# Optimization experiments

Hardware: AMD Instinct MI355X
Metric: run time of the kernel (lower is better)

The kernel has to match this reference:

```python
import jax, jax.numpy as jnp
import numpy as np

# dims: B=4 batch, S=512 seq, P=128 input_size, C=64 classes(=hidden_size), K=64 gln layer width, 4 context bits -> 16 contexts
B, S, P, C, K, NBITS = 4, 512, 128, 64, 64, 4
NCTX = 2 ** NBITS
LOGIT_CLIP = 5.0


def setup_inputs() -> dict:
    key = jax.random.key(0)
    ks = jax.random.split(key, 8)
    return {
        "x": jax.random.normal(ks[0], (B, S, P), jnp.float32),
        "hidden": jax.random.normal(ks[1], (B, C), jnp.float32),
        # GLN layer 1: per-class, per-neuron halfspace context hyperplanes and gated weights
        "H1": jax.random.normal(ks[2], (C, K, NBITS, P), jnp.float32),
        "W1": jax.random.normal(ks[3], (C, K, NCTX, P), jnp.float32) / np.sqrt(P),
        # GLN output layer: one neuron per class
        "H2": jax.random.normal(ks[4], (C, NBITS, P), jnp.float32),
        "W2": jax.random.normal(ks[5], (C, NCTX, K), jnp.float32) / np.sqrt(K),
        # fc2: Linear(input_size, hidden_size)
        "fc2_w": jax.random.normal(ks[6], (C, P), jnp.float32) / np.sqrt(P),
        "fc2_b": jnp.zeros((C,), jnp.float32),
    }


def _ctx_index(bits):
    # bits: (..., NBITS) bool -> integer context id in [0, 2^NBITS)
    return (bits * (2 ** jnp.arange(NBITS, dtype=jnp.int32))).sum(-1)


def _gln_predict(x, H1, W1, H2, W2):
    # base predictions: sigmoid(x) -> logit space is x itself (clipped for stability)
    l0 = jnp.clip(x, -LOGIT_CLIP, LOGIT_CLIP)  # (B,S,P)
    # layer 1: halfspace gating then geometric mixing in logit space
    ctx1 = _ctx_index(jnp.einsum('bsp,ckjp->bsckj', x, H1) > 0)          # (B,S,C,K)
    mix1 = jnp.einsum('bsp,ckxp->bsckx', l0, W1)                          # (B,S,C,K,NCTX)
    l1 = jnp.take_along_axis(mix1, ctx1[..., None], axis=-1)[..., 0]      # (B,S,C,K)
    l1 = jnp.clip(l1, -LOGIT_CLIP, LOGIT_CLIP)
    # output layer: one gated neuron per class
    ctx2 = _ctx_index(jnp.einsum('bsp,cjp->bscj', x, H2) > 0)             # (B,S,C)
    mix2 = jnp.einsum('bsck,cxk->bscx', l1, W2)                           # (B,S,C,NCTX)
    l2 = jnp.take_along_axis(mix2, ctx2[..., None], axis=-1)[..., 0]      # (B,S,C)
    return jax.nn.sigmoid(l2)


def reference(x, hidden, H1, W1, H2, W2, fc2_w, fc2_b):
    b = _gln_predict(x, H1, W1, H2, W2)                   # (B,S,C)
    # multihead gating
    sig_alphas = jax.nn.sigmoid(x @ fc2_w.T + fc2_b)      # (B,S,C)
    b = b * sig_alphas

    # sequential roll+add+relu recurrence over seq_len
    def step(h, bt):
        h = jax.nn.relu(bt + jnp.roll(h, 1, axis=-1))
        return h, h

    h_last, outs = jax.lax.scan(step, hidden, jnp.swapaxes(b, 0, 1))  # outs: (S,B,C)
    outputs = jnp.swapaxes(outs, 0, 1)                                # (B,S,C)
    return outputs, h_last
```

## Files before the change

### kernel.cpp

```cpp
#include <hip/hip_runtime.h>
#include <math.h>

#define BB 4
#define SS 512
#define PP 128
#define CC 64
#define KK 64
#define NCTX_ 16
#define TT 64
#define NTILES ((BB*SS)/TT)

typedef __attribute__((ext_vector_type(8))) short bf16x8;
typedef __attribute__((ext_vector_type(4))) float f32x4;

static __device__ __forceinline__ float bf2f(short h) {
    unsigned u = ((unsigned)(unsigned short)h) << 16;
    return __builtin_bit_cast(float, u);
}
static __device__ __forceinline__ short f2bf(float f) {
    unsigned u = __builtin_bit_cast(unsigned, f);
    unsigned r = (u + 0x7fffu + ((u >> 16) & 1u)) >> 16;
    return (short)(unsigned short)r;
}
static __device__ __forceinline__ bf16x8 clampfrag(bf16x8 h) {
    typedef __attribute__((ext_vector_type(4))) unsigned u32x4;
    u32x4 u = __builtin_bit_cast(u32x4, h);
    #pragma unroll
    for (int i = 0; i < 4; ++i) {
        const unsigned w = u[i];
        const unsigned s = w & 0x80008000u;
        unsigned lo = w & 0x7fffu;
        unsigned hi = (w >> 16) & 0x7fffu;
        lo = lo > 0x40a0u ? 0x40a0u : lo;
        hi = hi > 0x40a0u ? 0x40a0u : hi;
        u[i] = s | lo | (hi << 16);
    }
    return __builtin_bit_cast(bf16x8, u);
}

__global__ __launch_bounds__(256) void h1pack_kernel(const float* __restrict__ H1,
                                                     short* __restrict__ H1h,
                                                     short* __restrict__ H1l)
{
    const int lane = threadIdx.x & 63;
    const int gw   = blockIdx.x * 4 + (threadIdx.x >> 6);
    const int row  = (gw >> 2) * 16 + (lane >> 2);
    const int col  = (gw & 3) * 32 + (lane & 3) * 8;
    const float4* src = reinterpret_cast<const float4*>(H1 + (size_t)row * PP + col);
    const float4 v0 = src[0], v1 = src[1];
    const float vv[8] = {v0.x, v0.y, v0.z, v0.w, v1.x, v1.y, v1.z, v1.w};
    bf16x8 hh, ll;
    #pragma unroll
    for (int e = 0; e < 8; ++e) {
        const short hv = f2bf(vv[e]);
        hh[e] = hv;
        ll[e] = f2bf(vv[e] - bf2f(hv));
    }
    const int lp = (lane & 3) * 16 + (lane >> 2);
    const size_t o = ((size_t)gw * 64 + lp) * 8;
    *reinterpret_cast<bf16x8*>(H1h + o) = hh;
    *reinterpret_cast<bf16x8*>(H1l + o) = ll;
}

__global__ __launch_bounds__(256) void w1pack_kernel(const float* __restrict__ W1,
                                                     short* __restrict__ W1h)
{
    const int lane = threadIdx.x & 63;
    const int q    = threadIdx.x >> 6;
    const int tile = blockIdx.x;
    const float4* src = reinterpret_cast<const float4*>(
        W1 + ((size_t)tile * 16 + (lane >> 2)) * PP + q * 32 + (lane & 3) * 8);
    const float4 v0 = src[0], v1 = src[1];
    const float vv[8] = {v0.x, v0.y, v0.z, v0.w, v1.x, v1.y, v1.z, v1.w};
    bf16x8 hh;
    #pragma unroll
    for (int e = 0; e < 8; ++e) hh[e] = f2bf(vv[e]);
    const int lp = (lane & 3) * 16 + (lane >> 2);
    const size_t o = (((size_t)tile * 4 + q) * 64 + lp) * 8;
    *reinterpret_cast<bf16x8*>(W1h + o) = hh;
}

__global__ __launch_bounds__(256) void h2wpack_kernel(const float* __restrict__ H2,
                                                      const float* __restrict__ fc2w,
                                                      short* __restrict__ Hh,
                                                      short* __restrict__ Hl)
{
    const int cidx = blockIdx.x;
    const int q    = threadIdx.x >> 6;
    const int l    = threadIdx.x & 63;
    const int row  = l & 15;
    const int col  = q * 32 + (l >> 4) * 8;
    float vv[8];
    if (row < 4) {
        const float4* s = reinterpret_cast<const float4*>(
            H2 + ((size_t)cidx * 4 + row) * PP + col);
        const float4 a = s[0], b = s[1];
        vv[0]=a.x; vv[1]=a.y; vv[2]=a.z; vv[3]=a.w;
        vv[4]=b.x; vv[5]=b.y; vv[6]=b.z; vv[7]=b.w;
    } else if (row == 4) {
        const float4* s = reinterpret_cast<const float4*>(
            fc2w + (size_t)cidx * PP + col);
        const float4 a = s[0], b = s[1];
        vv[0]=a.x; vv[1]=a.y; vv[2]=a.z; vv[3]=a.w;
        vv[4]=b.x; vv[5]=b.y; vv[6]=b.z; vv[7]=b.w;
    } else {
        #pragma unroll
        for (int e = 0; e < 8; ++e) vv[e] = 0.f;
    }
    bf16x8 hh, ll;
    #pragma unroll
    for (int e = 0; e < 8; ++e) {
        const short hv = f2bf(vv[e]);
        hh[e] = hv;
        ll[e] = f2bf(vv[e] - bf2f(hv));
    }
    const size_t o = (((size_t)cidx * 4 + q) * 64 + l) * 8;
    *reinterpret_cast<bf16x8*>(Hh + o) = hh;
    *reinterpret_cast<bf16x8*>(Hl + o) = ll;
}

__global__ __launch_bounds__(256, 4) void predict_kernel(
    const float* __restrict__ x,
    const short* __restrict__ H1h,
    const short* __restrict__ H1l,
    const short* __restrict__ W1h,
    const short* __restrict__ H2Wh,
    const short* __restrict__ H2Wl,
    const float* __restrict__ W2,
    const float* __restrict__ fc2b,
    float* __restrict__ bout)
{
    __shared__ short xuh[4][4][64][8];
    __shared__ short xul[4][4][64][8];
    __shared__ unsigned char ctxb[TT][68];
    __shared__ unsigned char bit2b[TT];
    __shared__ float af[TT];

    const int tid  = threadIdx.x;
    const int lane = tid & 63;
    const int wid  = __builtin_amdgcn_readfirstlane(tid >> 6);
    const int bid  = blockIdx.x;
    const int sw   = ((bid & 7) << 8) | (bid >> 3);
    const int c    = sw >> 5;
    const int tile = sw & (NTILES - 1);
    const int tok0 = tile * TT;

    const int t15 = lane & 15;
    const int g   = lane >> 4;
    const f32x4 zero4 = {0.f, 0.f, 0.f, 0.f};

    {
        const int tok = tid >> 2;
        const int q   = tid & 3;
        const int tl  = tok & 15;
        const int jj  = tok >> 4;
        const float4* x4 = reinterpret_cast<const float4*>(
            x + (size_t)(tok0 + tok) * PP + q * 32);
        float v[32];
        #pragma unroll
        for (int i = 0; i < 8; ++i) {
            const float4 t = x4[i];
            v[i*4+0]=t.x; v[i*4+1]=t.y; v[i*4+2]=t.z; v[i*4+3]=t.w;
        }
        #pragma unroll
        for (int gg = 0; gg < 4; ++gg) {
            bf16x8 hh, ll;
            #pragma unroll
            for (int e = 0; e < 8; ++e) {
                const float f = v[gg*8+e];
                const short hv = f2bf(f);
                hh[e] = hv;
                ll[e] = f2bf(f - bf2f(hv));
            }
            *reinterpret_cast<bf16x8*>(&xuh[jj][q][gg*16 + tl][0]) = hh;
            *reinterpret_cast<bf16x8*>(&xul[jj][q][gg*16 + tl][0]) = ll;
        }
    }
    __syncthreads();

    const int ctile = c * 16 + wid * 4;
    #pragma unroll
    for (int half = 0; half < 2; ++half) {
        f32x4 acc[4][2];
        #pragma unroll
        for (int nt = 0; nt < 4; ++nt) { acc[nt][0] = zero4; acc[nt][1] = zero4; }
        #pragma unroll
        for (int q = 0; q < 4; ++q) {
            bf16x8 bh[2], bl[2];
            #pragma unroll
            for (int j2 = 0; j2 < 2; ++j2) {
                const int j = half * 2 + j2;
                bh[j2] = *reinterpret_cast<const bf16x8*>(&xuh[j][q][lane][0]);
                bl[j2] = *reinterpret_cast<const bf16x8*>(&xul[j][q][lane][0]);
            }
            #pragma unroll
            for (int nt = 0; nt < 4; ++nt) {
                const size_t fo = (((size_t)(ctile + nt) * 4 + q) * 64 + lane) * 8;
                const bf16x8 ah = *reinterpret_cast<const bf16x8*>(H1h + fo);
                const bf16x8 al = *reinterpret_cast<const bf16x8*>(H1l + fo);
                #pragma unroll
                for (int j2 = 0; j2 < 2; ++j2) {
                    acc[nt][j2] = __builtin_amdgcn_mfma_f32_16x16x32_bf16(ah, bh[j2], acc[nt][j2], 0, 0, 0);
                    acc[nt][j2] = __builtin_amdgcn_mfma_f32_16x16x32_bf16(ah, bl[j2], acc[nt][j2], 0, 0, 0);
                    acc[nt][j2] = __builtin_amdgcn_mfma_f32_16x16x32_bf16(al, bh[j2], acc[nt][j2], 0, 0, 0);
                }
            }
        }
        #pragma unroll
        for (int nt = 0; nt < 4; ++nt) {
            #pragma unroll
            for (int j2 = 0; j2 < 2; ++j2) {
                const int tok = half * 32 + j2 * 16 + t15;
                const int k   = wid * 16 + nt * 4 + g;
                const int cv  = (acc[nt][j2][0] > 0.f ? 1 : 0) |
                                (acc[nt][j2][1] > 0.f ? 2 : 0) |
                                (acc[nt][j2][2] > 0.f ? 4 : 0) |
                                (acc[nt][j2][3] > 0.f ? 8 : 0);
                ctxb[tok][k] = (unsigned char)cv;
            }
        }
    }

    {
        f32x4 a2 = zero4;
        #pragma unroll
        for (int q = 0; q < 4; ++q) {
            const bf16x8 bh = *reinterpret_cast<const bf16x8*>(&xuh[wid][q][lane][0]);
            const bf16x8 bl = *reinterpret_cast<const bf16x8*>(&xul[wid][q][lane][0]);
            const size_t fo = (((size_t)(c * 4 + q)) * 64 + lane) * 8;
            const bf16x8 ah = *reinterpret_cast<const bf16x8*>(H2Wh + fo);
            const bf16x8 al = *reinterpret_cast<const bf16x8*>(H2Wl + fo);
            a2 = __builtin_amdgcn_mfma_f32_16x16x32_bf16(ah, bh, a2, 0, 0, 0);
            a2 = __builtin_amdgcn_mfma_f32_16x16x32_bf16(ah, bl, a2, 0, 0, 0);
            a2 = __builtin_amdgcn_mfma_f32_16x16x32_bf16(al, bh, a2, 0, 0, 0);
        }
        const int tok = wid * 16 + t15;
        if (g == 0) {
            bit2b[tok] = (unsigned char)((a2[0] > 0.f ? 1 : 0) | (a2[1] > 0.f ? 2 : 0) |
                                         (a2[2] > 0.f ? 4 : 0) | (a2[3] > 0.f ? 8 : 0));
        } else if (g == 1) {
            af[tok] = a2[0];
        }
    }
    __syncthreads();

    short* l1s = &xul[0][0][0][0];
    {
        bf16x8 ch[4][4];
        #pragma unroll
        for (int j = 0; j < 4; ++j)
            #pragma unroll
            for (int q = 0; q < 4; ++q)
                ch[j][q] = clampfrag(*reinterpret_cast<const bf16x8*>(&xuh[j][q][lane][0]));

        #pragma unroll 4
        for (int k16 = 0; k16 < 16; ++k16) {
            const int k = wid * 16 + k16;
            f32x4 acc[4] = {zero4, zero4, zero4, zero4};
            #pragma unroll
            for (int q = 0; q < 4; ++q) {
                const size_t fo = (((size_t)(c * KK + k) * 4 + q) * 64 + lane) * 8;
                const bf16x8 ah = *reinterpret_cast<const bf16x8*>(W1h + fo);
                #pragma unroll
                for (int j = 0; j < 4; ++j)
                    acc[j] = __builtin_amdgcn_mfma_f32_16x16x32_bf16(ah, ch[j][q], acc[j], 0, 0, 0);
            }
            #pragma unroll
            for (int j = 0; j < 4; ++j) {
                const int tok = j * 16 + t15;
                const int cx  = ctxb[tok][k];
                const int sel = cx & 3;
                const float v = (sel == 0) ? acc[j][0] : (sel == 1) ? acc[j][1] :
                                (sel == 2) ? acc[j][2] : acc[j][3];
                if (g == (cx >> 2))
                    l1s[tok * 68 + k] = f2bf(fminf(fmaxf(v, -5.f), 5.f));
            }
        }
    }
    __syncthreads();

    {
        const int tok = tid >> 2;
        const int qt  = tid & 3;
        const int ctx2 = bit2b[tok];
        const float4* w2p = reinterpret_cast<const float4*>(
            W2 + ((size_t)c * NCTX_ + ctx2) * KK + qt * 16);
        float s = 0.f;
        #pragma unroll
        for (int i4 = 0; i4 < 4; ++i4) {
            const float4 w = w2p[i4];
            const int kb = tok * 68 + qt * 16 + i4 * 4;
            s = fmaf(w.x, bf2f(l1s[kb + 0]),
                fmaf(w.y, bf2f(l1s[kb + 1]),
                fmaf(w.z, bf2f(l1s[kb + 2]),
                fmaf(w.w, bf2f(l1s[kb + 3]), s))));
        }
        s += __shfl_xor(s, 1, 64);
        s += __shfl_xor(s, 2, 64);
        if (qt == 0) {
            const float alpha = af[tok] + fc2b[c];
            const float bv = (1.f / (1.f + expf(-s))) * (1.f / (1.f + expf(-alpha)));
            bout[(size_t)(tok0 + tok) * CC + c] = bv;
        }
    }
}

__global__ __launch_bounds__(256, 4) void predict_fb_kernel(
    const float* __restrict__ x,
    const float* __restrict__ H1,
    const float* __restrict__ W1b,
    const float* __restrict__ H2,
    const float* __restrict__ W2,
    const float* __restrict__ fc2w,
    const float* __restrict__ fc2b,
    float* __restrict__ bout)
{
    __shared__ float xs[PP][TT + 1];
    __shared__ float bitss[4][TT];
    __shared__ float apart[4][TT];
    __shared__ float l2part[4][TT];

    const int tid  = threadIdx.x;
    const int lane = tid & 63;
    const int wid  = __builtin_amdgcn_readfirstlane(tid >> 6);
    const int bid  = blockIdx.x;
    const int sw   = ((bid & 7) << 8) | (bid >> 3);
    const int c    = sw >> 5;
    const int tile = sw & (NTILES - 1);
    const int tok0 = tile * TT;

    {
        const float4* xg = reinterpret_cast<const float4*>(x + (size_t)tok0 * PP);
        #pragma unroll
        for (int it = 0; it < (TT * PP / 4) / 256; ++it) {
            const int i = it * 256 + tid;
            const float4 v = xg[i];
            const int t = i >> 5;
            const int p = (i & 31) << 2;
            xs[p + 0][t] = v.x; xs[p + 1][t] = v.y;
            xs[p + 2][t] = v.z; xs[p + 3][t] = v.w;
        }
    }
    __syncthreads();

    int ctxreg[16];
    {
        const float4* H1c4 = reinterpret_cast<const float4*>(H1 + (size_t)c * KK * 4 * PP);
        #pragma unroll
        for (int gg = 0; gg < 8; ++gg) {
            const int k = wid * 16 + gg * 2;
            const float4* h4 = H1c4 + (size_t)k * 4 * 32;
            float acc[8] = {0.f, 0.f, 0.f, 0.f, 0.f, 0.f, 0.f, 0.f};
            #pragma unroll 2
            for (int p4 = 0; p4 < 32; ++p4) {
                const float x0 = xs[4 * p4 + 0][lane];
                const float x1 = xs[4 * p4 + 1][lane];
                const float x2 = xs[4 * p4 + 2][lane];
                const float x3 = xs[4 * p4 + 3][lane];
                #pragma unroll
                for (int r = 0; r < 8; ++r) {
                    const float4 w = h4[r * 32 + p4];
                    acc[r] = fmaf(w.w, x3, fmaf(w.z, x2, fmaf(w.y, x1, fmaf(w.x, x0, acc[r]))));
                }
            }
            ctxreg[gg * 2]     = (acc[0] > 0.f ? 1 : 0) | (acc[1] > 0.f ? 2 : 0) |
                                 (acc[2] > 0.f ? 4 : 0) | (acc[3] > 0.f ? 8 : 0);
            ctxreg[gg * 2 + 1] = (acc[4] > 0.f ? 1 : 0) | (acc[5] > 0.f ? 2 : 0) |
                                 (acc[6] > 0.f ? 4 : 0) | (acc[7] > 0.f ? 8 : 0);
        }
    }
    {
        const float4* h2 = reinterpret_cast<const float4*>(H2 + ((size_t)c * 4 + wid) * PP);
        float d = 0.f;
        #pragma unroll 8
        for (int p4 = 0; p4 < 32; ++p4) {
            const float4 w = h2[p4];
            d = fmaf(w.w, xs[4 * p4 + 3][lane], fmaf(w.z, xs[4 * p4 + 2][lane],
                fmaf(w.y, xs[4 * p4 + 1][lane], fmaf(w.x, xs[4 * p4 + 0][lane], d))));
        }
        bitss[wid][lane] = (d > 0.f) ? 1.f : 0.f;
        const float4* fw = reinterpret_cast<const float4*>(fc2w + (size_t)c * PP) + wid * 8;
        float ap = 0.f;
        #pragma unroll
        for (int p4 = 0; p4 < 8; ++p4) {
            const float4 w = fw[p4];
            const int p = wid * 32 + 4 * p4;
            ap = fmaf(w.w, xs[p + 3][lane], fmaf(w.z, xs[p + 2][lane],
                 fmaf(w.y, xs[p + 1][lane], fmaf(w.x, xs[p + 0][lane], ap))));
        }
        apart[wid][lane] = ap;
    }
    __syncthreads();

    float l1v[16];
    {
        const float4* W1c4 = reinterpret_cast<const float4*>(W1b) +
                             (size_t)(c * KK + wid * 16) * 512;
        #pragma unroll
        for (int gg = 0; gg < 2; ++gg) {
            float s[8] = {0.f, 0.f, 0.f, 0.f, 0.f, 0.f, 0.f, 0.f};
            const float4* wp[8];
            #pragma unroll
            for (int jj = 0; jj < 8; ++jj) {
                const int kk = gg * 8 + jj;
                wp[jj] = W1c4 + (size_t)kk * 512 + (size_t)ctxreg[kk] * 32;
            }
            #pragma unroll 2
            for (int p4 = 0; p4 < 32; ++p4) {
                const float x0 = fminf(fmaxf(xs[4 * p4 + 0][lane], -5.f), 5.f);
                const float x1 = fminf(fmaxf(xs[4 * p4 + 1][lane], -5.f), 5.f);
                const float x2 = fminf(fmaxf(xs[4 * p4 + 2][lane], -5.f), 5.f);
                const float x3 = fminf(fmaxf(xs[4 * p4 + 3][lane], -5.f), 5.f);
                #pragma unroll
                for (int jj = 0; jj < 8; ++jj) {
                    const float4 wv = wp[jj][p4];
                    s[jj] = fmaf(wv.w, x3, fmaf(wv.z, x2, fmaf(wv.y, x1, fmaf(wv.x, x0, s[jj]))));
                }
            }
            #pragma unroll
            for (int jj = 0; jj < 8; ++jj)
                l1v[gg * 8 + jj] = fminf(fmaxf(s[jj], -5.f), 5.f);
        }
    }
    {
        const int ctx2 = (bitss[0][lane] > 0.5f ? 1 : 0) | (bitss[1][lane] > 0.5f ? 2 : 0) |
                         (bitss[2][lane] > 0.5f ? 4 : 0) | (bitss[3][lane] > 0.5f ? 8 : 0);
        const float* w2 = W2 + ((size_t)c * NCTX_ + ctx2) * KK + wid * 16;
        float lp = 0.f;
        #pragma unroll
        for (int jj = 0; jj < 16; ++jj) lp = fmaf(w2[jj], l1v[jj], lp);
        l2part[wid][lane] = lp;
    }
    __syncthreads();
    if (wid == 0) {
        const int t = lane;
        const float l2 = (l2part[0][t] + l2part[1][t]) + (l2part[2][t] + l2part[3][t]);
        const float alpha = apart[0][t] + apart[1][t] + apart[2][t] + apart[3][t] + fc2b[c];
        const float bv = (1.f / (1.f + expf(-l2))) * (1.f / (1.f + expf(-alpha)));
        bout[(size_t)(tok0 + t) * CC + c] = bv;
    }
}

__global__ __launch_bounds__(64) void scan_kernel(const float* __restrict__ hidden,
                                                  float* __restrict__ out)
{
    const int b    = blockIdx.x;
    const int lane = threadIdx.x;
    float* row = out + (size_t)b * SS * CC;
    const float hprev = hidden[b * CC + ((lane + 63) & 63)];

    float nb[64];
    #pragma unroll
    for (int j = 0; j < 64; ++j) nb[j] = row[j * CC + ((lane + j) & 63)];
    float acc = fmaxf(nb[0] + hprev, 0.f);
    row[lane] = acc;
    #pragma unroll
    for (int j = 1; j < 64; ++j) {
        acc += nb[j];
        row[j * CC + ((lane + j) & 63)] = acc;
    }
    for (int c0 = 64; c0 < SS; c0 += 64) {
        #pragma unroll
        for (int j = 0; j < 64; ++j)
            nb[j] = row[(c0 + j) * CC + ((lane + c0 + j) & 63)];
        #pragma unroll
        for (int j = 0; j < 64; ++j) {
            acc += nb[j];
            row[(c0 + j) * CC + ((lane + c0 + j) & 63)] = acc;
        }
    }
    out[(size_t)BB * SS * CC + b * CC + ((lane + 63) & 63)] = acc;
}

extern "C" void kernel_launch(void* const* d_in, const int* in_sizes, int n_in,
                              void* d_out, int out_size, void* d_ws, size_t ws_size,
                              hipStream_t stream) {
    const float* x      = (const float*)d_in[0];
    const float* hidden = (const float*)d_in[1];
    const float* H1     = (const float*)d_in[2];
    const float* W1     = (const float*)d_in[3];
    const float* H2     = (const float*)d_in[4];
    const float* W2     = (const float*)d_in[5];
    const float* fc2w   = (const float*)d_in[6];
    const float* fc2b   = (const float*)d_in[7];
    float* out = (float*)d_out;

    const size_t MB = 1024 * 1024;

    if (ws_size >= 25 * MB) {
        short* W1hp = (short*)d_ws;
        short* H1hp = (short*)((char*)d_ws + 16 * MB);
        short* H1lp = (short*)((char*)d_ws + 20 * MB);
        short* H2Whp = (short*)((char*)d_ws + 24 * MB);
        short* H2Wlp = (short*)((char*)d_ws + 24 * MB + 256 * 1024);
        w1pack_kernel<<<dim3(CC * KK), 256, 0, stream>>>(W1, W1hp);
        h1pack_kernel<<<dim3(1024), 256, 0, stream>>>(H1, H1hp, H1lp);
        h2wpack_kernel<<<dim3(CC), 256, 0, stream>>>(H2, fc2w, H2Whp, H2Wlp);
        predict_kernel<<<dim3(CC * NTILES), 256, 0, stream>>>(
            x, H1hp, H1lp, W1hp, H2Whp, H2Wlp, W2, fc2b, out);
    } else {
        predict_fb_kernel<<<dim3(CC * NTILES), 256, 0, stream>>>(
            x, H1, W1, H2, W2, fc2w, fc2b, out);
    }
    scan_kernel<<<dim3(BB), 64, 0, stream>>>(hidden, out);
}
```

Before: 110.2 us.

## Use 32x32x16 MFMA for gating projections and merge pack kernels into one launch

The H1 and H2/fc2 gating projections move from 16x16x32 to 32x32x16 bf16 MFMA tiles. The shared-memory x fragments and the packed H1/H2 weight layouts are reorganised to match, and the W1 path re-indexes into the new layout. The three weight-packing kernels become a single launch, cutting launch overhead and making fewer, larger MFMA calls. In exchange the accumulators are larger (16 floats each), which raises register pressure under the occupancy-4 launch bound, and the H2 projection now runs on only two of the four waves.

```diff
diff --git a/kernel.cpp b/kernel.cpp
--- a/kernel.cpp
+++ b/kernel.cpp
@@ -12,6 +12,7 @@
 
 typedef __attribute__((ext_vector_type(8))) short bf16x8;
 typedef __attribute__((ext_vector_type(4))) float f32x4;
+typedef __attribute__((ext_vector_type(16))) float f32x16;
 
 static __device__ __forceinline__ float bf2f(short h) {
     unsigned u = ((unsigned)(unsigned short)h) << 16;
@@ -38,91 +39,87 @@
     return __builtin_bit_cast(bf16x8, u);
 }
 
-__global__ __launch_bounds__(256) void h1pack_kernel(const float* __restrict__ H1,
-                                                     short* __restrict__ H1h,
-                                                     short* __restrict__ H1l)
+__global__ __launch_bounds__(256) void pack_kernel(
+    const float* __restrict__ W1, const float* __restrict__ H1,
+    const float* __restrict__ H2, const float* __restrict__ fc2w,
+    short* __restrict__ W1h, short* __restrict__ H1h32, short* __restrict__ H1l32,
+    short* __restrict__ H2Wh, short* __restrict__ H2Wl)
 {
+    const int bid  = blockIdx.x;
+    const int w    = threadIdx.x >> 6;
     const int lane = threadIdx.x & 63;
-    const int gw   = blockIdx.x * 4 + (threadIdx.x >> 6);
-    const int row  = (gw >> 2) * 16 + (lane >> 2);
-    const int col  = (gw & 3) * 32 + (lane & 3) * 8;
-    const float4* src = reinterpret_cast<const float4*>(H1 + (size_t)row * PP + col);
-    const float4 v0 = src[0], v1 = src[1];
-    const float vv[8] = {v0.x, v0.y, v0.z, v0.w, v1.x, v1.y, v1.z, v1.w};
-    bf16x8 hh, ll;
-    #pragma unroll
-    for (int e = 0; e < 8; ++e) {
-        const short hv = f2bf(vv[e]);
-        hh[e] = hv;
-        ll[e] = f2bf(vv[e] - bf2f(hv));
-    }
-    const int lp = (lane & 3) * 16 + (lane >> 2);
-    const size_t o = ((size_t)gw * 64 + lp) * 8;
-    *reinterpret_cast<bf16x8*>(H1h + o) = hh;
-    *reinterpret_cast<bf16x8*>(H1l + o) = ll;
-}
-
-__global__ __launch_bounds__(256) void w1pack_kernel(const float* __restrict__ W1,
-                                                     short* __restrict__ W1h)
-{
-    const int lane = threadIdx.x & 63;
-    const int q    = threadIdx.x >> 6;
-    const int tile = blockIdx.x;
-    const float4* src = reinterpret_cast<const float4*>(
-        W1 + ((size_t)tile * 16 + (lane >> 2)) * PP + q * 32 + (lane & 3) * 8);
-    const float4 v0 = src[0], v1 = src[1];
-    const float vv[8] = {v0.x, v0.y, v0.z, v0.w, v1.x, v1.y, v1.z, v1.w};
-    bf16x8 hh;
-    #pragma unroll
-    for (int e = 0; e < 8; ++e) hh[e] = f2bf(vv[e]);
-    const int lp = (lane & 3) * 16 + (lane >> 2);
-    const size_t o = (((size_t)tile * 4 + q) * 64 + lp) * 8;
-    *reinterpret_cast<bf16x8*>(W1h + o) = hh;
-}
-
-__global__ __launch_bounds__(256) void h2wpack_kernel(const float* __restrict__ H2,
-                                                      const float* __restrict__ fc2w,
-                                                      short* __restrict__ Hh,
-                                                      short* __restrict__ Hl)
-{
-    const int cidx = blockIdx.x;
-    const int q    = threadIdx.x >> 6;
-    const int l    = threadIdx.x & 63;
-    const int row  = l & 15;
-    const int col  = q * 32 + (l >> 4) * 8;
-    float vv[8];
-    if (row < 4) {
-        const float4* s = reinterpret_cast<const float4*>(
-            H2 + ((size_t)cidx * 4 + row) * PP + col);
+
+    if (bid < CC * KK) {
+        const int tile = bid;
+        const int q    = w;
+        const float4* src = reinterpret_cast<const float4*>(
+            W1 + ((size_t)tile * 16 + (lane >> 2)) * PP + q * 32 + (lane & 3) * 8);
+        const float4 v0 = src[0], v1 = src[1];
+        const float vv[8] = {v0.x, v0.y, v0.z, v0.w, v1.x, v1.y, v1.z, v1.w};
+        bf16x8 hh;
+        #pragma unroll
+        for (int e = 0; e < 8; ++e) hh[e] = f2bf(vv[e]);
+        const int lp = (lane & 3) * 16 + (lane >> 2);
+        *reinterpret_cast<bf16x8*>(W1h + (((size_t)tile * 4 + q) * 64 + lp) * 8) = hh;
+    } else if (bid < CC * KK + 1024) {
+        const int gw  = (bid - CC * KK) * 4 + w;
+        const int row = (gw >> 3) * 32 + (lane & 31);
+        const int col = (gw & 7) * 16 + (lane >> 5) * 8;
+        const float4* s = reinterpret_cast<const float4*>(H1 + (size_t)row * PP + col);
         const float4 a = s[0], b = s[1];
-        vv[0]=a.x; vv[1]=a.y; vv[2]=a.z; vv[3]=a.w;
-        vv[4]=b.x; vv[5]=b.y; vv[6]=b.z; vv[7]=b.w;
-    } else if (row == 4) {
-        const float4* s = reinterpret_cast<const float4*>(
-            fc2w + (size_t)cidx * PP + col);
-        const float4 a = s[0], b = s[1];
-        vv[0]=a.x; vv[1]=a.y; vv[2]=a.z; vv[3]=a.w;
-        vv[4]=b.x; vv[5]=b.y; vv[6]=b.z; vv[7]=b.w;
+        const float vv[8] = {a.x, a.y, a.z, a.w, b.x, b.y, b.z, b.w};
+        bf16x8 hh, ll;
+        #pragma unroll
+        for (int e = 0; e < 8; ++e) {
+            const short hv = f2bf(vv[e]);
+            hh[e] = hv;
+            ll[e] = f2bf(vv[e] - bf2f(hv));
+        }
+        const size_t o = ((size_t)gw * 64 + lane) * 8;
+        *reinterpret_cast<bf16x8*>(H1h32 + o) = hh;
+        *reinterpret_cast<bf16x8*>(H1l32 + o) = ll;
     } else {
-        #pragma unroll
-        for (int e = 0; e < 8; ++e) vv[e] = 0.f;
-    }
-    bf16x8 hh, ll;
-    #pragma unroll
-    for (int e = 0; e < 8; ++e) {
-        const short hv = f2bf(vv[e]);
-        hh[e] = hv;
-        ll[e] = f2bf(vv[e] - bf2f(hv));
-    }
-    const size_t o = (((size_t)cidx * 4 + q) * 64 + l) * 8;
-    *reinterpret_cast<bf16x8*>(Hh + o) = hh;
-    *reinterpret_cast<bf16x8*>(Hl + o) = ll;
+        const int cidx = bid - (CC * KK + 1024);
+        #pragma unroll
+        for (int i = 0; i < 2; ++i) {
+            const int q8  = w * 2 + i;
+            const int row = lane & 31;
+            const int col = q8 * 16 + (lane >> 5) * 8;
+            float vv[8];
+            if (row < 4) {
+                const float4* s = reinterpret_cast<const float4*>(
+                    H2 + ((size_t)cidx * 4 + row) * PP + col);
+                const float4 a = s[0], b = s[1];
+                vv[0]=a.x; vv[1]=a.y; vv[2]=a.z; vv[3]=a.w;
+                vv[4]=b.x; vv[5]=b.y; vv[6]=b.z; vv[7]=b.w;
+            } else if (row == 4) {
+                const float4* s = reinterpret_cast<const float4*>(
+                    fc2w + (size_t)cidx * PP + col);
+                const float4 a = s[0], b = s[1];
+                vv[0]=a.x; vv[1]=a.y; vv[2]=a.z; vv[3]=a.w;
+                vv[4]=b.x; vv[5]=b.y; vv[6]=b.z; vv[7]=b.w;
+            } else {
+                #pragma unroll
+                for (int e = 0; e < 8; ++e) vv[e] = 0.f;
+            }
+            bf16x8 hh, ll;
+            #pragma unroll
+            for (int e = 0; e < 8; ++e) {
+                const short hv = f2bf(vv[e]);
+                hh[e] = hv;
+                ll[e] = f2bf(vv[e] - bf2f(hv));
+            }
+            const size_t o = (((size_t)cidx * 8 + q8) * 64 + lane) * 8;
+            *reinterpret_cast<bf16x8*>(H2Wh + o) = hh;
+            *reinterpret_cast<bf16x8*>(H2Wl + o) = ll;
+        }
+    }
 }
 
 __global__ __launch_bounds__(256, 4) void predict_kernel(
     const float* __restrict__ x,
-    const short* __restrict__ H1h,
-    const short* __restrict__ H1l,
+    const short* __restrict__ H1h32,
+    const short* __restrict__ H1l32,
     const short* __restrict__ W1h,
     const short* __restrict__ H2Wh,
     const short* __restrict__ H2Wl,
@@ -130,8 +127,8 @@
     const float* __restrict__ fc2b,
     float* __restrict__ bout)
 {
-    __shared__ short xuh[4][4][64][8];
-    __shared__ short xul[4][4][64][8];
+    __shared__ short xuh[2][8][64][8];
+    __shared__ short xul[2][8][64][8];
     __shared__ unsigned char ctxb[TT][68];
     __shared__ unsigned char bit2b[TT];
     __shared__ float af[TT];
@@ -147,15 +144,18 @@
 
     const int t15 = lane & 15;
     const int g   = lane >> 4;
-    const f32x4 zero4 = {0.f, 0.f, 0.f, 0.f};
+    const int l31 = lane & 31;
+    const int l5  = lane >> 5;
+    const f32x4  zero4  = {0.f, 0.f, 0.f, 0.f};
+    const f32x16 zero16 = {0.f,0.f,0.f,0.f,0.f,0.f,0.f,0.f,
+                           0.f,0.f,0.f,0.f,0.f,0.f,0.f,0.f};
 
     {
         const int tok = tid >> 2;
-        const int q   = tid & 3;
-        const int tl  = tok & 15;
-        const int jj  = tok >> 4;
+        const int qq  = tid & 3;
+        const int ct  = tok >> 5;
         const float4* x4 = reinterpret_cast<const float4*>(
-            x + (size_t)(tok0 + tok) * PP + q * 32);
+            x + (size_t)(tok0 + tok) * PP + qq * 32);
         float v[32];
         #pragma unroll
         for (int i = 0; i < 8; ++i) {
@@ -164,6 +164,8 @@
         }
         #pragma unroll
         for (int gg = 0; gg < 4; ++gg) {
+            const int q8 = qq * 2 + (gg >> 1);
+            const int lw = (gg & 1) * 32 + (tok & 31);
             bf16x8 hh, ll;
             #pragma unroll
             for (int e = 0; e < 8; ++e) {
@@ -172,73 +174,62 @@
                 hh[e] = hv;
                 ll[e] = f2bf(f - bf2f(hv));
             }
-            *reinterpret_cast<bf16x8*>(&xuh[jj][q][gg*16 + tl][0]) = hh;
-            *reinterpret_cast<bf16x8*>(&xul[jj][q][gg*16 + tl][0]) = ll;
-        }
-    }
-    __syncthreads();
-
-    const int ctile = c * 16 + wid * 4;
+            *reinterpret_cast<bf16x8*>(&xuh[ct][q8][lw][0]) = hh;
+            *reinterpret_cast<bf16x8*>(&xul[ct][q8][lw][0]) = ll;
+        }
+    }
+    __syncthreads();
+
     #pragma unroll
-    for (int half = 0; half < 2; ++half) {
-        f32x4 acc[4][2];
-        #pragma unroll
-        for (int nt = 0; nt < 4; ++nt) { acc[nt][0] = zero4; acc[nt][1] = zero4; }
-        #pragma unroll
-        for (int q = 0; q < 4; ++q) {
-            bf16x8 bh[2], bl[2];
-            #pragma unroll
-            for (int j2 = 0; j2 < 2; ++j2) {
-                const int j = half * 2 + j2;
-                bh[j2] = *reinterpret_cast<const bf16x8*>(&xuh[j][q][lane][0]);
-                bl[j2] = *reinterpret_cast<const bf16x8*>(&xul[j][q][lane][0]);
-            }
-            #pragma unroll
-            for (int nt = 0; nt < 4; ++nt) {
-                const size_t fo = (((size_t)(ctile + nt) * 4 + q) * 64 + lane) * 8;
-                const bf16x8 ah = *reinterpret_cast<const bf16x8*>(H1h + fo);
-                const bf16x8 al = *reinterpret_cast<const bf16x8*>(H1l + fo);
-                #pragma unroll
-                for (int j2 = 0; j2 < 2; ++j2) {
-                    acc[nt][j2] = __builtin_amdgcn_mfma_f32_16x16x32_bf16(ah, bh[j2], acc[nt][j2], 0, 0, 0);
-                    acc[nt][j2] = __builtin_amdgcn_mfma_f32_16x16x32_bf16(ah, bl[j2], acc[nt][j2], 0, 0, 0);
-                    acc[nt][j2] = __builtin_amdgcn_mfma_f32_16x16x32_bf16(al, bh[j2], acc[nt][j2], 0, 0, 0);
-                }
-            }
-        }
-        #pragma unroll
-        for (int nt = 0; nt < 4; ++nt) {
-            #pragma unroll
-            for (int j2 = 0; j2 < 2; ++j2) {
-                const int tok = half * 32 + j2 * 16 + t15;
-                const int k   = wid * 16 + nt * 4 + g;
-                const int cv  = (acc[nt][j2][0] > 0.f ? 1 : 0) |
-                                (acc[nt][j2][1] > 0.f ? 2 : 0) |
-                                (acc[nt][j2][2] > 0.f ? 4 : 0) |
-                                (acc[nt][j2][3] > 0.f ? 8 : 0);
-                ctxb[tok][k] = (unsigned char)cv;
-            }
-        }
-    }
-
-    {
-        f32x4 a2 = zero4;
-        #pragma unroll
-        for (int q = 0; q < 4; ++q) {
-            const bf16x8 bh = *reinterpret_cast<const bf16x8*>(&xuh[wid][q][lane][0]);
-            const bf16x8 bl = *reinterpret_cast<const bf16x8*>(&xul[wid][q][lane][0]);
-            const size_t fo = (((size_t)(c * 4 + q)) * 64 + lane) * 8;
+    for (int rt = 0; rt < 2; ++rt) {
+        f32x16 aA = zero16, aB = zero16;
+        const size_t tb = ((size_t)(c * 8 + wid * 2 + rt)) * 8;
+        #pragma unroll
+        for (int q8 = 0; q8 < 8; ++q8) {
+            const size_t fo = ((tb + q8) * 64 + lane) * 8;
+            const bf16x8 ah  = *reinterpret_cast<const bf16x8*>(H1h32 + fo);
+            const bf16x8 al  = *reinterpret_cast<const bf16x8*>(H1l32 + fo);
+            const bf16x8 bh0 = *reinterpret_cast<const bf16x8*>(&xuh[0][q8][lane][0]);
+            const bf16x8 bl0 = *reinterpret_cast<const bf16x8*>(&xul[0][q8][lane][0]);
+            const bf16x8 bh1 = *reinterpret_cast<const bf16x8*>(&xuh[1][q8][lane][0]);
+            const bf16x8 bl1 = *reinterpret_cast<const bf16x8*>(&xul[1][q8][lane][0]);
+            aA = __builtin_amdgcn_mfma_f32_32x32x16_bf16(ah, bh0, aA, 0, 0, 0);
+            aA = __builtin_amdgcn_mfma_f32_32x32x16_bf16(ah, bl0, aA, 0, 0, 0);
+            aA = __builtin_amdgcn_mfma_f32_32x32x16_bf16(al, bh0, aA, 0, 0, 0);
+            aB = __builtin_amdgcn_mfma_f32_32x32x16_bf16(ah, bh1, aB, 0, 0, 0);
+            aB = __builtin_amdgcn_mfma_f32_32x32x16_bf16(ah, bl1, aB, 0, 0, 0);
+            aB = __builtin_amdgcn_mfma_f32_32x32x16_bf16(al, bh1, aB, 0, 0, 0);
+        }
+        #pragma unroll
+        for (int rg = 0; rg < 4; ++rg) {
+            const int k = wid * 16 + rt * 8 + 2 * rg + l5;
+            const int cvA = (aA[4*rg+0] > 0.f ? 1 : 0) | (aA[4*rg+1] > 0.f ? 2 : 0) |
+                            (aA[4*rg+2] > 0.f ? 4 : 0) | (aA[4*rg+3] > 0.f ? 8 : 0);
+            const int cvB = (aB[4*rg+0] > 0.f ? 1 : 0) | (aB[4*rg+1] > 0.f ? 2 : 0) |
+                            (aB[4*rg+2] > 0.f ? 4 : 0) | (aB[4*rg+3] > 0.f ? 8 : 0);
+            ctxb[l31][k]      = (unsigned char)cvA;
+            ctxb[32 + l31][k] = (unsigned char)cvB;
+        }
+    }
+
+    if (wid < 2) {
+        f32x16 a2 = zero16;
+        #pragma unroll
+        for (int q8 = 0; q8 < 8; ++q8) {
+            const size_t fo = (((size_t)c * 8 + q8) * 64 + lane) * 8;
             const bf16x8 ah = *reinterpret_cast<const bf16x8*>(H2Wh + fo);
             const bf16x8 al = *reinterpret_cast<const bf16x8*>(H2Wl + fo);
-            a2 = __builtin_amdgcn_mfma_f32_16x16x32_bf16(ah, bh, a2, 0, 0, 0);
-            a2 = __builtin_amdgcn_mfma_f32_16x16x32_bf16(ah, bl, a2, 0, 0, 0);
-            a2 = __builtin_amdgcn_mfma_f32_16x16x32_bf16(al, bh, a2, 0, 0, 0);
-        }
-        const int tok = wid * 16 + t15;
-        if (g == 0) {
+            const bf16x8 bh = *reinterpret_cast<const bf16x8*>(&xuh[wid][q8][lane][0]);
+            const bf16x8 bl = *reinterpret_cast<const bf16x8*>(&xul[wid][q8][lane][0]);
+            a2 = __builtin_amdgcn_mfma_f32_32x32x16_bf16(ah, bh, a2, 0, 0, 0);
+            a2 = __builtin_amdgcn_mfma_f32_32x32x16_bf16(ah, bl, a2, 0, 0, 0);
+            a2 = __builtin_amdgcn_mfma_f32_32x32x16_bf16(al, bh, a2, 0, 0, 0);
+        }
+        const int tok = wid * 32 + l31;
+        if (l5 == 0) {
             bit2b[tok] = (unsigned char)((a2[0] > 0.f ? 1 : 0) | (a2[1] > 0.f ? 2 : 0) |
                                          (a2[2] > 0.f ? 4 : 0) | (a2[3] > 0.f ? 8 : 0));
-        } else if (g == 1) {
+        } else {
             af[tok] = a2[0];
         }
     }
@@ -250,8 +241,11 @@
         #pragma unroll
         for (int j = 0; j < 4; ++j)
             #pragma unroll
-            for (int q = 0; q < 4; ++q)
-                ch[j][q] = clampfrag(*reinterpret_cast<const bf16x8*>(&xuh[j][q][lane][0]));
+            for (int q = 0; q < 4; ++q) {
+                const int q8 = 2 * q + (g >> 1);
+                const int lw = (g & 1) * 32 + (j & 1) * 16 + t15;
+                ch[j][q] = clampfrag(*reinterpret_cast<const bf16x8*>(&xuh[j >> 1][q8][lw][0]));
+            }
 
         #pragma unroll 4
         for (int k16 = 0; k16 < 16; ++k16) {
@@ -488,14 +482,13 @@
     const size_t MB = 1024 * 1024;
 
     if (ws_size >= 25 * MB) {
-        short* W1hp = (short*)d_ws;
-        short* H1hp = (short*)((char*)d_ws + 16 * MB);
-        short* H1lp = (short*)((char*)d_ws + 20 * MB);
+        short* W1hp  = (short*)d_ws;
+        short* H1hp  = (short*)((char*)d_ws + 16 * MB);
+        short* H1lp  = (short*)((char*)d_ws + 20 * MB);
         short* H2Whp = (short*)((char*)d_ws + 24 * MB);
-        short* H2Wlp = (short*)((char*)d_ws + 24 * MB + 256 * 1024);
-        w1pack_kernel<<<dim3(CC * KK), 256, 0, stream>>>(W1, W1hp);
-        h1pack_kernel<<<dim3(1024), 256, 0, stream>>>(H1, H1hp, H1lp);
-        h2wpack_kernel<<<dim3(CC), 256, 0, stream>>>(H2, fc2w, H2Whp, H2Wlp);
+        short* H2Wlp = (short*)((char*)d_ws + 24 * MB + 512 * 1024);
+        pack_kernel<<<dim3(CC * KK + 1024 + CC), 256, 0, stream>>>(
+            W1, H1, H2, fc2w, W1hp, H1hp, H1lp, H2Whp, H2Wlp);
         predict_kernel<<<dim3(CC * NTILES), 256, 0, stream>>>(
             x, H1hp, H1lp, W1hp, H2Whp, H2Wlp, W2, fc2b, out);
     } else {
```

Result: faster. 104.4 us (-5.3%).
